# Kernel optimization log

Hardware: AMD Instinct MI355X
Metric: run time of the kernel (lower is better)

## Reference

```python
import jax, jax.numpy as jnp
import numpy as np

B, L, V, H = 4096, 80, 256, 512  # batch, NLE_TERM_CO, charset, msg_hdim


def setup_inputs() -> dict:
    key = jax.random.key(0)
    k0, k1, k2 = jax.random.split(key, 3)
    message = jax.random.randint(k0, (B, L), 0, V, dtype=jnp.int64)
    # Linear(i_dim=L*V, H): store weight as [L*V, H] (i.e. torch weight.T)
    W1 = jax.random.normal(k1, (L * V, H), dtype=jnp.float32) * 0.01
    b1 = jnp.zeros((H,), dtype=jnp.float32)
    W2 = jax.random.normal(k2, (H, H), dtype=jnp.float32) * 0.02
    b2 = jnp.zeros((H,), dtype=jnp.float32)
    return {"message": message, "W1": W1, "b1": b1, "W2": W2, "b2": b2}


def reference(message, W1, b1, W2, b2):
    # one_hot(message, 256).reshape(B, L*256) @ W1  ==  gather rows of W1 at
    # flat index pos*256 + char, summed over positions (no one-hot materialized).
    idx = message + jnp.arange(L, dtype=message.dtype)[None, :] * V  # [B, L]
    emb = jnp.take(W1, idx, axis=0).sum(axis=1)                       # [B, H]
    h = jax.nn.relu(emb + b1)
    out = jax.nn.relu(h @ W2 + b2)
    return out
```

## Files before the change

### kernel.cpp

```cpp
#include <hip/hip_runtime.h>
#include <hip/hip_bf16.h>
#include <stdint.h>

#define B_ 4096
#define L_ 80
#define V_ 256
#define H_ 512

typedef __attribute__((ext_vector_type(4))) float f32x4;
typedef __attribute__((ext_vector_type(8))) short bf16x8;
typedef __attribute__((ext_vector_type(8))) unsigned short ushort8;

static __device__ __forceinline__ unsigned short f2bf(float x) {
  union { float f; unsigned int u; } a;
  a.f = x;
  unsigned int r = a.u + 0x7fffu + ((a.u >> 16) & 1u);
  return (unsigned short)(r >> 16);
}
static __device__ __forceinline__ float bf2f(unsigned short u) {
  union { unsigned int i; float f; } a;
  a.i = ((unsigned int)u) << 16;
  return a.f;
}

__global__ __launch_bounds__(256) void prep(
    const float* __restrict__ W2, const float* __restrict__ W1,
    unsigned short* __restrict__ W2T, unsigned short* __restrict__ W1b) {
  const int bid = blockIdx.x;
  if (bid < 256) {
    __shared__ float tile[32][33];
    const int ti = bid & 15, tj = bid >> 4;
    const int r = threadIdx.x >> 5, c = threadIdx.x & 31;
#pragma unroll
    for (int rr = r; rr < 32; rr += 8)
      tile[rr][c] = W2[(size_t)(ti * 32 + rr) * H_ + tj * 32 + c];
    __syncthreads();
#pragma unroll
    for (int rr = r; rr < 32; rr += 8)
      W2T[(size_t)(tj * 32 + rr) * H_ + ti * 32 + c] = f2bf(tile[c][rr]);
  } else {
    const size_t i8 = ((size_t)(bid - 256) * 256 + threadIdx.x) * 8;
    f32x4 v0 = *reinterpret_cast<const f32x4*>(W1 + i8);
    f32x4 v1 = *reinterpret_cast<const f32x4*>(W1 + i8 + 4);
    ushort8 o;
    o[0] = f2bf(v0[0]); o[1] = f2bf(v0[1]); o[2] = f2bf(v0[2]); o[3] = f2bf(v0[3]);
    o[4] = f2bf(v1[0]); o[5] = f2bf(v1[1]); o[6] = f2bf(v1[2]); o[7] = f2bf(v1[3]);
    *reinterpret_cast<ushort8*>(W1b + i8) = o;
  }
}

__global__ __launch_bounds__(512) void encode_gather_bf(
    const int* __restrict__ msg, const unsigned short* __restrict__ W1b,
    const float* __restrict__ b1, unsigned short* __restrict__ h) {
  const int BT = 16;
  __shared__ int offs[BT * L_];
  const int t = threadIdx.x;
  const int b0 = blockIdx.x * BT;
  const int w = t >> 6;
  const int lane = t & 63;
  const int c8 = lane * 8;

  for (int i = t; i < BT * L_; i += 512) {
    int b = i / L_, l = i - b * L_;
    offs[i] = (l * V_ + msg[(b0 + b) * L_ + l]) * H_;
  }
  __syncthreads();

  const int r0 = w * 2, r1 = r0 + 1;
  float a0[8] = {}, a1[8] = {};

#pragma unroll 4
  for (int l = 0; l < L_; ++l) {
    int o0 = __builtin_amdgcn_readfirstlane(offs[r0 * L_ + l]);
    int o1 = __builtin_amdgcn_readfirstlane(offs[r1 * L_ + l]);
    ushort8 v0 = *reinterpret_cast<const ushort8*>(W1b + o0 + c8);
    ushort8 v1 = *reinterpret_cast<const ushort8*>(W1b + o1 + c8);
#pragma unroll
    for (int j = 0; j < 8; ++j) {
      a0[j] += bf2f(v0[j]);
      a1[j] += bf2f(v1[j]);
    }
  }

  ushort8 o0, o1;
#pragma unroll
  for (int j = 0; j < 8; ++j) {
    float bias = b1[c8 + j];
    float x0 = a0[j] + bias, x1 = a1[j] + bias;
    o0[j] = f2bf(x0 > 0.f ? x0 : 0.f);
    o1[j] = f2bf(x1 > 0.f ? x1 : 0.f);
  }
  *reinterpret_cast<ushort8*>(&h[(size_t)(b0 + r0) * H_ + c8]) = o0;
  *reinterpret_cast<ushort8*>(&h[(size_t)(b0 + r1) * H_ + c8]) = o1;
}

__global__ __launch_bounds__(512) void encode_gather_f32(
    const int* __restrict__ msg, const float* __restrict__ W1,
    const float* __restrict__ b1, unsigned short* __restrict__ h) {
  const int BT = 16;
  __shared__ int offs[BT * L_];
  const int t = threadIdx.x;
  const int b0 = blockIdx.x * BT;
  const int g = t >> 7;
  const int c4 = (t & 127) * 4;

  for (int i = t; i < BT * L_; i += 512) {
    int b = i / L_, l = i - b * L_;
    offs[i] = (l * V_ + msg[(b0 + b) * L_ + l]) * H_;
  }
  __syncthreads();

  f32x4 acc[4] = {};
#pragma unroll 2
  for (int l = 0; l < L_; ++l) {
#pragma unroll
    for (int rr = 0; rr < 4; ++rr) {
      int o = __builtin_amdgcn_readfirstlane(offs[(g * 4 + rr) * L_ + l]);
      acc[rr] += *reinterpret_cast<const f32x4*>(W1 + o + c4);
    }
  }
  const f32x4 bias = *reinterpret_cast<const f32x4*>(b1 + c4);
#pragma unroll
  for (int rr = 0; rr < 4; ++rr) {
    f32x4 v = acc[rr] + bias;
    ushort4 o;
    o.x = f2bf(v[0] > 0.f ? v[0] : 0.f);
    o.y = f2bf(v[1] > 0.f ? v[1] : 0.f);
    o.z = f2bf(v[2] > 0.f ? v[2] : 0.f);
    o.w = f2bf(v[3] > 0.f ? v[3] : 0.f);
    *reinterpret_cast<ushort4*>(&h[(size_t)(b0 + g * 4 + rr) * H_ + c4]) = o;
  }
}

__global__ __launch_bounds__(256) void gemm_out(
    const unsigned short* __restrict__ h, const unsigned short* __restrict__ W2T,
    const float* __restrict__ b2, float* __restrict__ out) {
  const int wid = threadIdx.x >> 6;
  const int lane = threadIdx.x & 63;
  const int wm = wid >> 1, wn = wid & 1;
  const int bm = blockIdx.x * 64;
  const int bn = blockIdx.y * 64;
  const int lr = lane & 15;
  const int lq = lane >> 4;

  f32x4 acc[2][2] = {};

  const unsigned short* aptr = h + (size_t)(bm + wm * 32 + lr) * H_ + lq * 8;
  const unsigned short* bptr = W2T + (size_t)(bn + wn * 32 + lr) * H_ + lq * 8;

#pragma unroll 2
  for (int kt = 0; kt < H_ / 32; ++kt) {
    const int ko = kt * 32;
    bf16x8 a[2], bb[2];
#pragma unroll
    for (int mi = 0; mi < 2; ++mi)
      a[mi] = *reinterpret_cast<const bf16x8*>(aptr + (size_t)mi * 16 * H_ + ko);
#pragma unroll
    for (int ni = 0; ni < 2; ++ni)
      bb[ni] = *reinterpret_cast<const bf16x8*>(bptr + (size_t)ni * 16 * H_ + ko);
#pragma unroll
    for (int mi = 0; mi < 2; ++mi)
#pragma unroll
      for (int ni = 0; ni < 2; ++ni)
        acc[mi][ni] = __builtin_amdgcn_mfma_f32_16x16x32_bf16(
            a[mi], bb[ni], acc[mi][ni], 0, 0, 0);
  }

#pragma unroll
  for (int mi = 0; mi < 2; ++mi) {
#pragma unroll
    for (int ni = 0; ni < 2; ++ni) {
      const int n = bn + wn * 32 + ni * 16 + lr;
      const float bias = b2[n];
#pragma unroll
      for (int r = 0; r < 4; ++r) {
        const int m = bm + wm * 32 + mi * 16 + lq * 4 + r;
        float v = acc[mi][ni][r] + bias;
        out[(size_t)m * H_ + n] = v > 0.f ? v : 0.f;
      }
    }
  }
}

extern "C" void kernel_launch(void* const* d_in, const int* in_sizes, int n_in,
                              void* d_out, int out_size, void* d_ws, size_t ws_size,
                              hipStream_t stream) {
  const int* msg   = (const int*)d_in[0];
  const float* W1  = (const float*)d_in[1];
  const float* b1  = (const float*)d_in[2];
  const float* W2  = (const float*)d_in[3];
  const float* b2  = (const float*)d_in[4];
  float* out = (float*)d_out;

  const size_t W2T_OFF = 0;
  const size_t H_OFF   = (size_t)H_ * H_ * 2;
  const size_t W1B_OFF = H_OFF + (size_t)B_ * H_ * 2;
  const size_t NEED    = W1B_OFF + (size_t)L_ * V_ * H_ * 2;

  unsigned short* W2T = (unsigned short*)((char*)d_ws + W2T_OFF);
  unsigned short* h   = (unsigned short*)((char*)d_ws + H_OFF);
  unsigned short* W1b = (unsigned short*)((char*)d_ws + W1B_OFF);

  if (ws_size >= NEED) {
    const int conv_blocks = (L_ * V_ * H_) / (256 * 8);
    hipLaunchKernelGGL(prep, dim3(256 + conv_blocks), dim3(256), 0, stream,
                       W2, W1, W2T, W1b);
    hipLaunchKernelGGL(encode_gather_bf, dim3(B_ / 16), dim3(512), 0, stream,
                       msg, W1b, b1, h);
  } else {
    const int conv_blocks = 0;
    hipLaunchKernelGGL(prep, dim3(256 + conv_blocks), dim3(256), 0, stream,
                       W2, W1, W2T, W1b);
    hipLaunchKernelGGL(encode_gather_f32, dim3(B_ / 16), dim3(512), 0, stream,
                       msg, W1, b1, h);
  }

  hipLaunchKernelGGL(gemm_out, dim3(B_ / 64, H_ / 64), dim3(256), 0, stream,
                     h, W2T, b2, out);
}
```

Measured before the change: 140.8 us.

## Fuse gather-embed and output GEMM into one kernel via LDS-staged hidden tile

Merges the gather/sum encoder and the W2 GEMM into a single kernel. Each block keeps its 16-row bf16 hidden tile in padded LDS, then its 8 waves each compute 64 output columns with MFMA. This removes the global round trip of h and one kernel launch, and drops the fp32 fallback path so the workspace is assumed large enough. The cost is that every block rereads all of W2T (mostly from cache) and the GEMM runs with a small M tile of 16. The prep kernel now orders W1 conversion blocks before the W2 transpose blocks.

New measurement: 128.7 us. 1.09x faster.

```diff
diff --git a/kernel.cpp b/kernel.cpp
--- a/kernel.cpp
+++ b/kernel.cpp
@@ -6,6 +6,8 @@
 #define L_ 80
 #define V_ 256
 #define H_ 512
+#define BT 16
+#define HP 520
 
 typedef __attribute__((ext_vector_type(4))) float f32x4;
 typedef __attribute__((ext_vector_type(8))) short bf16x8;
@@ -27,9 +29,18 @@
     const float* __restrict__ W2, const float* __restrict__ W1,
     unsigned short* __restrict__ W2T, unsigned short* __restrict__ W1b) {
   const int bid = blockIdx.x;
-  if (bid < 256) {
+  if (bid < 5120) {
+    const size_t i8 = ((size_t)bid * 256 + threadIdx.x) * 8;
+    f32x4 v0 = *reinterpret_cast<const f32x4*>(W1 + i8);
+    f32x4 v1 = *reinterpret_cast<const f32x4*>(W1 + i8 + 4);
+    ushort8 o;
+    o[0] = f2bf(v0[0]); o[1] = f2bf(v0[1]); o[2] = f2bf(v0[2]); o[3] = f2bf(v0[3]);
+    o[4] = f2bf(v1[0]); o[5] = f2bf(v1[1]); o[6] = f2bf(v1[2]); o[7] = f2bf(v1[3]);
+    *reinterpret_cast<ushort8*>(W1b + i8) = o;
+  } else {
     __shared__ float tile[32][33];
-    const int ti = bid & 15, tj = bid >> 4;
+    const int tb = bid - 5120;
+    const int ti = tb & 15, tj = tb >> 4;
     const int r = threadIdx.x >> 5, c = threadIdx.x & 31;
 #pragma unroll
     for (int rr = r; rr < 32; rr += 8)
@@ -38,27 +49,20 @@
 #pragma unroll
     for (int rr = r; rr < 32; rr += 8)
       W2T[(size_t)(tj * 32 + rr) * H_ + ti * 32 + c] = f2bf(tile[c][rr]);
-  } else {
-    const size_t i8 = ((size_t)(bid - 256) * 256 + threadIdx.x) * 8;
-    f32x4 v0 = *reinterpret_cast<const f32x4*>(W1 + i8);
-    f32x4 v1 = *reinterpret_cast<const f32x4*>(W1 + i8 + 4);
-    ushort8 o;
-    o[0] = f2bf(v0[0]); o[1] = f2bf(v0[1]); o[2] = f2bf(v0[2]); o[3] = f2bf(v0[3]);
-    o[4] = f2bf(v1[0]); o[5] = f2bf(v1[1]); o[6] = f2bf(v1[2]); o[7] = f2bf(v1[3]);
-    *reinterpret_cast<ushort8*>(W1b + i8) = o;
   }
 }
 
-__global__ __launch_bounds__(512) void encode_gather_bf(
+__global__ __launch_bounds__(512) void fused_gather_gemm(
     const int* __restrict__ msg, const unsigned short* __restrict__ W1b,
-    const float* __restrict__ b1, unsigned short* __restrict__ h) {
-  const int BT = 16;
+    const float* __restrict__ b1, const unsigned short* __restrict__ W2T,
+    const float* __restrict__ b2, float* __restrict__ out) {
   __shared__ int offs[BT * L_];
+  __shared__ unsigned short hl[BT * HP];
+
   const int t = threadIdx.x;
-  const int b0 = blockIdx.x * BT;
   const int w = t >> 6;
   const int lane = t & 63;
-  const int c8 = lane * 8;
+  const int b0 = blockIdx.x * BT;
 
   for (int i = t; i < BT * L_; i += 512) {
     int b = i / L_, l = i - b * L_;
@@ -66,7 +70,8 @@
   }
   __syncthreads();
 
-  const int r0 = w * 2, r1 = r0 + 1;
+  const int r0 = 2 * w, r1 = r0 + 1;
+  const int c8 = lane * 8;
   float a0[8] = {}, a1[8] = {};
 
 #pragma unroll 4
@@ -82,102 +87,43 @@
     }
   }
 
-  ushort8 o0, o1;
+  ushort8 h0, h1;
 #pragma unroll
   for (int j = 0; j < 8; ++j) {
     float bias = b1[c8 + j];
     float x0 = a0[j] + bias, x1 = a1[j] + bias;
-    o0[j] = f2bf(x0 > 0.f ? x0 : 0.f);
-    o1[j] = f2bf(x1 > 0.f ? x1 : 0.f);
+    h0[j] = f2bf(x0 > 0.f ? x0 : 0.f);
+    h1[j] = f2bf(x1 > 0.f ? x1 : 0.f);
   }
-  *reinterpret_cast<ushort8*>(&h[(size_t)(b0 + r0) * H_ + c8]) = o0;
-  *reinterpret_cast<ushort8*>(&h[(size_t)(b0 + r1) * H_ + c8]) = o1;
-}
-
-__global__ __launch_bounds__(512) void encode_gather_f32(
-    const int* __restrict__ msg, const float* __restrict__ W1,
-    const float* __restrict__ b1, unsigned short* __restrict__ h) {
-  const int BT = 16;
-  __shared__ int offs[BT * L_];
-  const int t = threadIdx.x;
-  const int b0 = blockIdx.x * BT;
-  const int g = t >> 7;
-  const int c4 = (t & 127) * 4;
-
-  for (int i = t; i < BT * L_; i += 512) {
-    int b = i / L_, l = i - b * L_;
-    offs[i] = (l * V_ + msg[(b0 + b) * L_ + l]) * H_;
-  }
+  *reinterpret_cast<ushort8*>(&hl[r0 * HP + c8]) = h0;
+  *reinterpret_cast<ushort8*>(&hl[r1 * HP + c8]) = h1;
   __syncthreads();
 
-  f32x4 acc[4] = {};
-#pragma unroll 2
-  for (int l = 0; l < L_; ++l) {
-#pragma unroll
-    for (int rr = 0; rr < 4; ++rr) {
-      int o = __builtin_amdgcn_readfirstlane(offs[(g * 4 + rr) * L_ + l]);
-      acc[rr] += *reinterpret_cast<const f32x4*>(W1 + o + c4);
-    }
-  }
-  const f32x4 bias = *reinterpret_cast<const f32x4*>(b1 + c4);
-#pragma unroll
-  for (int rr = 0; rr < 4; ++rr) {
-    f32x4 v = acc[rr] + bias;
-    ushort4 o;
-    o.x = f2bf(v[0] > 0.f ? v[0] : 0.f);
-    o.y = f2bf(v[1] > 0.f ? v[1] : 0.f);
-    o.z = f2bf(v[2] > 0.f ? v[2] : 0.f);
-    o.w = f2bf(v[3] > 0.f ? v[3] : 0.f);
-    *reinterpret_cast<ushort4*>(&h[(size_t)(b0 + g * 4 + rr) * H_ + c4]) = o;
-  }
-}
-
-__global__ __launch_bounds__(256) void gemm_out(
-    const unsigned short* __restrict__ h, const unsigned short* __restrict__ W2T,
-    const float* __restrict__ b2, float* __restrict__ out) {
-  const int wid = threadIdx.x >> 6;
-  const int lane = threadIdx.x & 63;
-  const int wm = wid >> 1, wn = wid & 1;
-  const int bm = blockIdx.x * 64;
-  const int bn = blockIdx.y * 64;
   const int lr = lane & 15;
   const int lq = lane >> 4;
+  f32x4 acc[4] = {};
 
-  f32x4 acc[2][2] = {};
+  const unsigned short* bp = W2T + (size_t)(w * 64 + lr) * H_ + lq * 8;
 
-  const unsigned short* aptr = h + (size_t)(bm + wm * 32 + lr) * H_ + lq * 8;
-  const unsigned short* bptr = W2T + (size_t)(bn + wn * 32 + lr) * H_ + lq * 8;
-
-#pragma unroll 2
+#pragma unroll 4
   for (int kt = 0; kt < H_ / 32; ++kt) {
-    const int ko = kt * 32;
-    bf16x8 a[2], bb[2];
+    bf16x8 a = *reinterpret_cast<const bf16x8*>(&hl[lr * HP + kt * 32 + lq * 8]);
 #pragma unroll
-    for (int mi = 0; mi < 2; ++mi)
-      a[mi] = *reinterpret_cast<const bf16x8*>(aptr + (size_t)mi * 16 * H_ + ko);
-#pragma unroll
-    for (int ni = 0; ni < 2; ++ni)
-      bb[ni] = *reinterpret_cast<const bf16x8*>(bptr + (size_t)ni * 16 * H_ + ko);
-#pragma unroll
-    for (int mi = 0; mi < 2; ++mi)
-#pragma unroll
-      for (int ni = 0; ni < 2; ++ni)
-        acc[mi][ni] = __builtin_amdgcn_mfma_f32_16x16x32_bf16(
-            a[mi], bb[ni], acc[mi][ni], 0, 0, 0);
+    for (int ni = 0; ni < 4; ++ni) {
+      bf16x8 b = *reinterpret_cast<const bf16x8*>(bp + (size_t)ni * 16 * H_ + kt * 32);
+      acc[ni] = __builtin_amdgcn_mfma_f32_16x16x32_bf16(a, b, acc[ni], 0, 0, 0);
+    }
   }
 
 #pragma unroll
-  for (int mi = 0; mi < 2; ++mi) {
+  for (int ni = 0; ni < 4; ++ni) {
+    const int n = w * 64 + ni * 16 + lr;
+    const float bias = b2[n];
 #pragma unroll
-    for (int ni = 0; ni < 2; ++ni) {
-      const int n = bn + wn * 32 + ni * 16 + lr;
-      const float bias = b2[n];
-#pragma unroll
-      for (int r = 0; r < 4; ++r) {
-        const int m = bm + wm * 32 + mi * 16 + lq * 4 + r;
-        float v = acc[mi][ni][r] + bias;
-        out[(size_t)m * H_ + n] = v > 0.f ? v : 0.f;
-      }
+    for (int r = 0; r < 4; ++r) {
+      const int m = lq * 4 + r;
+      float v = acc[ni][r] + bias;
+      out[(size_t)(b0 + m) * H_ + n] = v > 0.f ? v : 0.f;
     }
   }
 }
@@ -192,29 +138,11 @@
   const float* b2  = (const float*)d_in[4];
   float* out = (float*)d_out;
 
-  const size_t W2T_OFF = 0;
-  const size_t H_OFF   = (size_t)H_ * H_ * 2;
-  const size_t W1B_OFF = H_OFF + (size_t)B_ * H_ * 2;
-  const size_t NEED    = W1B_OFF + (size_t)L_ * V_ * H_ * 2;
+  unsigned short* W2T = (unsigned short*)d_ws;
+  unsigned short* W1b = (unsigned short*)((char*)d_ws + (size_t)H_ * H_ * 2);
 
-  unsigned short* W2T = (unsigned short*)((char*)d_ws + W2T_OFF);
-  unsigned short* h   = (unsigned short*)((char*)d_ws + H_OFF);
-  unsigned short* W1b = (unsigned short*)((char*)d_ws + W1B_OFF);
-
-  if (ws_size >= NEED) {
-    const int conv_blocks = (L_ * V_ * H_) / (256 * 8);
-    hipLaunchKernelGGL(prep, dim3(256 + conv_blocks), dim3(256), 0, stream,
-                       W2, W1, W2T, W1b);
-    hipLaunchKernelGGL(encode_gather_bf, dim3(B_ / 16), dim3(512), 0, stream,
-                       msg, W1b, b1, h);
-  } else {
-    const int conv_blocks = 0;
-    hipLaunchKernelGGL(prep, dim3(256 + conv_blocks), dim3(256), 0, stream,
-                       W2, W1, W2T, W1b);
-    hipLaunchKernelGGL(encode_gather_f32, dim3(B_ / 16), dim3(512), 0, stream,
-                       msg, W1, b1, h);
-  }
-
-  hipLaunchKernelGGL(gemm_out, dim3(B_ / 64, H_ / 64), dim3(256), 0, stream,
-                     h, W2T, b2, out);
+  hipLaunchKernelGGL(prep, dim3(5120 + 256), dim3(256), 0, stream,
+                     W2, W1, W2T, W1b);
+  hipLaunchKernelGGL(fused_gather_gemm, dim3(B_ / BT), dim3(512), 0, stream,
+                     msg, W1b, b1, W2T, b2, out);
 }
```
